# Kernel tuning notes

Measured on AMD Instinct MI355X. Metric: run time of the kernel, lower is better.

## Reference

```python
import jax, jax.numpy as jnp
import numpy as np

N = 50000      # nodes
E = 800000     # edges (before self loops)
IN = 256       # in_dim
HID = 32       # hidden_dim per head
H = 8          # heads layer 1
OUT = 64       # out_dim (classes)
NEG_SLOPE = 0.2  # PyG GATConv default


def gat_conv(x, ei, W, a_src, a_dst, b, heads, ch, concat):
    """PyG GATConv (eval mode, self-loops already in ei).
    x: [n, f_in], ei: [2, e] (row0=src j, row1=dst i), W: [f_in, heads*ch],
    a_src/a_dst: [heads, ch], b: [heads*ch] or [ch]."""
    n = x.shape[0]
    h = (x @ W).reshape(n, heads, ch)                      # [n, H, C]
    src, dst = ei[0], ei[1]
    alpha_src = (h * a_src).sum(-1)                        # [n, H]
    alpha_dst = (h * a_dst).sum(-1)                        # [n, H]
    e = jax.nn.leaky_relu(alpha_src[src] + alpha_dst[dst], NEG_SLOPE)  # [e, H]
    # segment softmax over incoming edges of each dst node
    emax = jax.lax.stop_gradient(jax.ops.segment_max(e, dst, num_segments=n))
    p = jnp.exp(e - emax[dst])
    denom = jax.ops.segment_sum(p, dst, num_segments=n)    # [n, H] (>0: self loops)
    alpha = p / denom[dst]                                 # [e, H]
    out = jax.ops.segment_sum(h[src] * alpha[:, :, None], dst, num_segments=n)  # [n, H, C]
    out = out.reshape(n, heads * ch) if concat else out.mean(axis=1)
    return out + b


def setup_inputs() -> dict:
    key = jax.random.key(0)
    ks = jax.random.split(key, 9)
    x = jax.random.normal(ks[0], (N, IN), jnp.float32)
    edge_index = jax.random.randint(ks[1], (2, E), 0, N, jnp.int32)
    W1 = jax.random.normal(ks[2], (IN, H * HID), jnp.float32) * 0.05
    a_src1 = jax.random.normal(ks[3], (H, HID), jnp.float32) * 0.1
    a_dst1 = jax.random.normal(ks[4], (H, HID), jnp.float32) * 0.1
    b1 = jnp.zeros((H * HID,), jnp.float32)
    W2 = jax.random.normal(ks[5], (H * HID, OUT), jnp.float32) * 0.05
    a_src2 = jax.random.normal(ks[6], (1, OUT), jnp.float32) * 0.1
    a_dst2 = jax.random.normal(ks[7], (1, OUT), jnp.float32) * 0.1
    b2 = jnp.zeros((OUT,), jnp.float32)
    return {"x": x, "edge_index": edge_index, "W1": W1, "a_src1": a_src1,
            "a_dst1": a_dst1, "b1": b1, "W2": W2, "a_src2": a_src2,
            "a_dst2": a_dst2, "b2": b2}


def reference(x, edge_index, W1, a_src1, a_dst1, b1, W2, a_src2, a_dst2, b2):
    n = x.shape[0]
    loops = jnp.arange(n, dtype=edge_index.dtype)
    ei = jnp.concatenate([edge_index, jnp.stack([loops, loops])], axis=1)  # add self loops
    h = gat_conv(x, ei, W1, a_src1, a_dst1, b1, H, HID, concat=True)
    h = jax.nn.relu(h)
    h = gat_conv(h, ei, W2, a_src2, a_dst2, b2, 1, OUT, concat=False)
    return jax.nn.log_softmax(h, axis=1)
```

## Files before the change

### kernel.cpp

```cpp
#include <hip/hip_runtime.h>
#include <math.h>

#define NNODES 50000
#define EORIG  800000
#define ETOT   850000
#define NBUCK  196
#define BSTRIDE 5120
#define P2CHUNK 4096
#define NBLK2  ((ETOT + P2CHUNK - 1)/P2CHUNK)

typedef __attribute__((ext_vector_type(8))) short bf8_t;
typedef __attribute__((ext_vector_type(4))) float f4_t;
typedef __attribute__((ext_vector_type(2))) float f2_t;

constexpr float LOG2E = 1.44269504f;

constexpr size_t align256(size_t x){ return (x + 255) & ~size_t(255); }
constexpr size_t OFF_OFFSETS = 0;
constexpr size_t OFF_DEG     = OFF_OFFSETS + align256((size_t)NNODES*4);
constexpr size_t OFF_GCUR    = OFF_DEG     + align256((size_t)NNODES*4);
constexpr size_t OFF_EPACK   = OFF_GCUR    + align256(NBUCK*4);
constexpr size_t OFF_SRC     = OFF_EPACK   + align256((size_t)NBUCK*BSTRIDE*4);
constexpr size_t OFF_AS1     = OFF_SRC     + align256((size_t)NBUCK*BSTRIDE*4);
constexpr size_t OFF_AD1     = OFF_AS1     + align256((size_t)NNODES*8*4);
constexpr size_t OFF_W1T     = OFF_AD1     + align256((size_t)NNODES*8*4);
constexpr size_t OFF_W2T     = OFF_W1T     + align256(256*256*2);
constexpr size_t OFF_H1F8    = OFF_W2T     + align256(64*256*2);
constexpr size_t OFF_OUT1B   = OFF_H1F8    + align256((size_t)NNODES*256);
constexpr size_t OFF_H2B     = OFF_H1F8;
constexpr size_t OFF_AS2     = OFF_OUT1B   + align256((size_t)NNODES*256*2);
constexpr size_t OFF_AD2     = OFF_AS2     + align256((size_t)NNODES*4);

__device__ __forceinline__ unsigned short f2bf(float f){
    union { float f; unsigned u; } v; v.f = f;
    unsigned r = v.u + 0x7FFF + ((v.u >> 16) & 1);
    return (unsigned short)(r >> 16);
}
__device__ __forceinline__ float bf2f(unsigned short s){
    union { unsigned u; float f; } v; v.u = ((unsigned)s) << 16;
    return v.f;
}


__global__ __launch_bounds__(256) void p3_part(const int* __restrict__ ei, int* __restrict__ gcur,
                                               int* __restrict__ epack){
    __shared__ int h[NBUCK];
    __shared__ int r[NBUCK];
    const int t = threadIdx.x;
    for (int i = t; i < NBUCK; i += 256){ h[i] = 0; r[i] = 0; }
    __syncthreads();
    const int base = blockIdx.x * P2CHUNK;
    int srcs[P2CHUNK/256], dsts[P2CHUNK/256];
#pragma unroll
    for (int j = 0; j < P2CHUNK/256; j++){
        int e = base + j*256 + t;
        if (e < ETOT){
            if (e < EORIG){ srcs[j] = ei[e]; dsts[j] = ei[EORIG + e]; }
            else          { srcs[j] = dsts[j] = e - EORIG; }
            atomicAdd(&h[dsts[j] >> 8], 1);
        } else dsts[j] = -1;
    }
    __syncthreads();
    for (int i = t; i < NBUCK; i += 256){
        int c = h[i];
        h[i] = c ? atomicAdd(&gcur[i], c) : 0;
    }
    __syncthreads();
#pragma unroll
    for (int j = 0; j < P2CHUNK/256; j++){
        if (dsts[j] >= 0){
            int b = dsts[j] >> 8;
            int rk = atomicAdd(&r[b], 1);
            epack[h[b] + rk] = (srcs[j] << 8) | (dsts[j] & 255);
        }
    }
}

__global__ __launch_bounds__(256) void p4_csr(const int* __restrict__ gcur, const int* __restrict__ epack,
                                              int* __restrict__ offsets, int* __restrict__ deg_g,
                                              int* __restrict__ srclist){
    __shared__ int deg[256];
    __shared__ int sm[256];
    __shared__ int cur[256];
    const int b = blockIdx.x, t = threadIdx.x;
    const int s0 = b * BSTRIDE, s1 = gcur[b];
    deg[t] = 0; __syncthreads();
    for (int i = s0 + t; i < s1; i += 256) atomicAdd(&deg[epack[i] & 255], 1);
    __syncthreads();
    int v = deg[t];
    sm[t] = v; __syncthreads();
    for (int off = 1; off < 256; off <<= 1){
        int add = (t >= off) ? sm[t-off] : 0;
        __syncthreads();
        sm[t] += add;
        __syncthreads();
    }
    int excl = sm[t] - v;
    int node = (b << 8) + t;
    if (node < NNODES){ offsets[node] = s0 + excl; deg_g[node] = v; }
    cur[t] = s0 + excl;
    __syncthreads();
    for (int i = s0 + t; i < s1; i += 256){
        int p = epack[i];
        int pos = atomicAdd(&cur[p & 255], 1);
        srclist[pos] = p >> 8;
    }
}


__global__ __launch_bounds__(256) void conv_w_k(const float* __restrict__ W1, const float* __restrict__ W2,
                                                short* __restrict__ w1t, short* __restrict__ w2t,
                                                int* __restrict__ gcur){
    int o = blockIdx.x*256 + threadIdx.x;
    if (o < NBUCK) gcur[o] = o * BSTRIDE;
    if (o < 256*256){
        int n = o >> 8, k = o & 255;
        w1t[o] = (short)f2bf(W1[k*256 + n]);
    } else {
        int o2 = o - 256*256;
        if (o2 < 64*256){
            int n = o2 >> 8, k = o2 & 255;
            w2t[o2] = (short)f2bf(W2[k*64 + n]);
        }
    }
}


__global__ __launch_bounds__(512) void gemm1_mfma(const float* __restrict__ x, const short* __restrict__ w1t,
        const float* __restrict__ a1s, const float* __restrict__ a1d,
        unsigned char* __restrict__ h1f8, float* __restrict__ as1, float* __restrict__ ad1){
    __shared__ short As[128][40];
    __shared__ short Bs[256][40];
    const int t = threadIdx.x;
    const int lane = t & 63, wave = t >> 6;
    const int wy = wave >> 2, wx = wave & 3;
    const int quad = lane >> 4, l15 = lane & 15;
    const int r0 = blockIdx.x * 128;
    const int srow = t >> 2, skoff = (t & 3) * 8;
    f4_t zero4 = {0.f,0.f,0.f,0.f};
    f4_t acc[4][4];
#pragma unroll
    for (int i=0;i<4;i++)
#pragma unroll
      for (int j=0;j<4;j++) acc[i][j] = zero4;

    for (int kk = 0; kk < 256; kk += 32){
        float4 xa0 = {0,0,0,0}, xa1 = {0,0,0,0};
        if (r0 + srow < NNODES){
            xa0 = *(const float4*)(x + (size_t)(r0+srow)*256 + kk + skoff);
            xa1 = *(const float4*)(x + (size_t)(r0+srow)*256 + kk + skoff + 4);
        }
        bf8_t b0  = *(const bf8_t*)(w1t + (size_t)(srow      )*256 + kk + skoff);
        bf8_t b1v = *(const bf8_t*)(w1t + (size_t)(srow + 128)*256 + kk + skoff);
        bf8_t a0;
        a0[0]=f2bf(xa0.x); a0[1]=f2bf(xa0.y); a0[2]=f2bf(xa0.z); a0[3]=f2bf(xa0.w);
        a0[4]=f2bf(xa1.x); a0[5]=f2bf(xa1.y); a0[6]=f2bf(xa1.z); a0[7]=f2bf(xa1.w);
        __syncthreads();
        *(bf8_t*)&As[srow     ][skoff] = a0;
        *(bf8_t*)&Bs[srow     ][skoff] = b0;
        *(bf8_t*)&Bs[srow+128][skoff] = b1v;
        __syncthreads();
        bf8_t af[4], bfr[4];
#pragma unroll
        for (int i=0;i<4;i++) af[i]  = *(const bf8_t*)&As[wy*64 + i*16 + l15][quad*8];
#pragma unroll
        for (int j=0;j<4;j++) bfr[j] = *(const bf8_t*)&Bs[wx*64 + j*16 + l15][quad*8];
#pragma unroll
        for (int i=0;i<4;i++)
#pragma unroll
          for (int j=0;j<4;j++)
            acc[i][j] = __builtin_amdgcn_mfma_f32_16x16x32_bf16(af[i], bfr[j], acc[i][j], 0,0,0);
    }
    const int colbase = wx*64;
    const int head0 = colbase >> 5;
    float cs[4], cd[4];
#pragma unroll
    for (int j=0;j<4;j++){
        cs[j] = a1s[colbase + j*16 + l15] * LOG2E;
        cd[j] = a1d[colbase + j*16 + l15] * LOG2E;
    }
#pragma unroll
    for (int i=0;i<4;i++){
        int rowb = r0 + wy*64 + i*16 + quad*4;
#pragma unroll
        for (int reg=0; reg<4; reg++){
            int row = rowb + reg;
            bool valid = row < NNODES;
            float sp0=0.f, dp0=0.f, sp1=0.f, dp1=0.f;
#pragma unroll
            for (int j=0;j<4;j++){
                float v = acc[i][j][reg];
                if (j < 2){ sp0 += v*cs[j]; dp0 += v*cd[j]; }
                else      { sp1 += v*cs[j]; dp1 += v*cd[j]; }
                if (valid){
                    unsigned enc = (unsigned)__builtin_amdgcn_cvt_pk_fp8_f32(v, v, 0, false);
                    h1f8[(size_t)row*256 + colbase + j*16 + l15] = (unsigned char)(enc & 0xffu);
                }
            }
            sp0 += __shfl_xor(sp0,1); sp0 += __shfl_xor(sp0,2); sp0 += __shfl_xor(sp0,4); sp0 += __shfl_xor(sp0,8);
            dp0 += __shfl_xor(dp0,1); dp0 += __shfl_xor(dp0,2); dp0 += __shfl_xor(dp0,4); dp0 += __shfl_xor(dp0,8);
            sp1 += __shfl_xor(sp1,1); sp1 += __shfl_xor(sp1,2); sp1 += __shfl_xor(sp1,4); sp1 += __shfl_xor(sp1,8);
            dp1 += __shfl_xor(dp1,1); dp1 += __shfl_xor(dp1,2); dp1 += __shfl_xor(dp1,4); dp1 += __shfl_xor(dp1,8);
            if (valid && l15 == 0){
                as1[row*8 + head0    ] = sp0;
                ad1[row*8 + head0    ] = dp0;
                as1[row*8 + head0 + 1] = sp1;
                ad1[row*8 + head0 + 1] = dp1;
            }
        }
    }
}


__global__ __launch_bounds__(256) void gemm2_mfma(const short* __restrict__ ab, const short* __restrict__ w2t,
        const float* __restrict__ a2s, const float* __restrict__ a2d,
        short* __restrict__ h2b, float* __restrict__ as2, float* __restrict__ ad2){
    __shared__ short As[128][40];
    __shared__ short Bs[64][40];
    const int t = threadIdx.x;
    const int lane = t & 63, wave = t >> 6;
    const int quad = lane >> 4, l15 = lane & 15;
    const int r0 = blockIdx.x * 128;
    const int srow = t >> 2, skoff = (t & 3) * 8;
    f4_t zero4 = {0.f,0.f,0.f,0.f};
    f4_t acc[2][4];
#pragma unroll
    for (int i=0;i<2;i++)
#pragma unroll
      for (int j=0;j<4;j++) acc[i][j] = zero4;

    for (int kk = 0; kk < 256; kk += 32){
        bf8_t a0 = {}, a1v = {};
        if (r0 + srow < NNODES)      a0  = *(const bf8_t*)(ab + (size_t)(r0+srow)*256 + kk + skoff);
        if (r0 + srow + 64 < NNODES) a1v = *(const bf8_t*)(ab + (size_t)(r0+srow+64)*256 + kk + skoff);
        bf8_t b0 = *(const bf8_t*)(w2t + (size_t)srow*256 + kk + skoff);
        __syncthreads();
        *(bf8_t*)&As[srow   ][skoff] = a0;
        *(bf8_t*)&As[srow+64][skoff] = a1v;
        *(bf8_t*)&Bs[srow   ][skoff] = b0;
        __syncthreads();
        bf8_t af[2], bfr[4];
#pragma unroll
        for (int i=0;i<2;i++) af[i]  = *(const bf8_t*)&As[wave*32 + i*16 + l15][quad*8];
#pragma unroll
        for (int j=0;j<4;j++) bfr[j] = *(const bf8_t*)&Bs[j*16 + l15][quad*8];
#pragma unroll
        for (int i=0;i<2;i++)
#pragma unroll
          for (int j=0;j<4;j++)
            acc[i][j] = __builtin_amdgcn_mfma_f32_16x16x32_bf16(af[i], bfr[j], acc[i][j], 0,0,0);
    }
    float cs[4], cd[4];
#pragma unroll
    for (int j=0;j<4;j++){
        cs[j] = a2s[j*16 + l15] * LOG2E;
        cd[j] = a2d[j*16 + l15] * LOG2E;
    }
#pragma unroll
    for (int i=0;i<2;i++){
        int rowb = r0 + wave*32 + i*16 + quad*4;
#pragma unroll
        for (int reg=0; reg<4; reg++){
            int row = rowb + reg;
            bool valid = row < NNODES;
            float sp=0.f, dp=0.f;
#pragma unroll
            for (int j=0;j<4;j++){
                float v = acc[i][j][reg];
                sp += v*cs[j]; dp += v*cd[j];
                if (valid) h2b[(size_t)row*64 + j*16 + l15] = (short)f2bf(v);
            }
            sp += __shfl_xor(sp,1); sp += __shfl_xor(sp,2); sp += __shfl_xor(sp,4); sp += __shfl_xor(sp,8);
            dp += __shfl_xor(dp,1); dp += __shfl_xor(dp,2); dp += __shfl_xor(dp,4); dp += __shfl_xor(dp,8);
            if (valid && l15 == 0){ as2[row] = sp; ad2[row] = dp; }
        }
    }
}


__global__ __launch_bounds__(256) void aggregate1_k(const unsigned char* __restrict__ h1f8,
        const float* __restrict__ as1, const float* __restrict__ ad1,
        const int* __restrict__ offsets, const int* __restrict__ deg_g,
        const int* __restrict__ srclist,
        const float* __restrict__ b1, short* __restrict__ out1b){
    int d = blockIdx.x*4 + (threadIdx.x >> 6);
    int lane = threadIdx.x & 63;
    if (d >= NNODES) return;
    const int sub    = lane >> 4;
    const int c16    = lane & 15;
    const int head_g = c16 >> 1;
    const int head_p = lane & 7;
    const int ep     = lane >> 3;
    int start = offsets[d];
    int deg = deg_g[d];
    float ad_p = ad1[d*8 + head_p];
    float denom = 0.f;
    f2_t acc[8];
#pragma unroll
    for (int i=0;i<8;i++) acc[i] = (f2_t){0.f,0.f};
    for (int w = 0; w < deg; w += 64){
        int deg_w = min(64, deg - w);
        int s_reg = srclist[start + w + min(lane, deg_w-1)];
        int ngr = (deg_w + 7) >> 3;
        auto comp_p = [&](int g)->float{
            int ei = g*8 + ep;
            int s  = __shfl(s_reg, min(ei, deg_w-1));
            float e = as1[s*8 + head_p] + ad_p;
            e = fmaxf(0.2f*e, e);
            float p = exp2f(e);
            return (ei < deg_w) ? p : 0.f;
        };
        float p_reg = comp_p(0);
        for (int g = 0; g < ngr; g++){
            float p_cur = p_reg;
            if (g + 1 < ngr) p_reg = comp_p(g+1);
#pragma unroll
            for (int q = 0; q < 2; q++){
                int eq = q*4 + sub;
                float pe = __shfl(p_cur, eq*8 + head_g);
                int   se = __shfl(s_reg, g*8 + eq);
                uint4 wv = *(const uint4*)(h1f8 + (size_t)se*256 + c16*16);
                f2_t v;
                v = __builtin_amdgcn_cvt_pk_f32_fp8(wv.x, false); acc[0] += pe*v;
                v = __builtin_amdgcn_cvt_pk_f32_fp8(wv.x, true);  acc[1] += pe*v;
                v = __builtin_amdgcn_cvt_pk_f32_fp8(wv.y, false); acc[2] += pe*v;
                v = __builtin_amdgcn_cvt_pk_f32_fp8(wv.y, true);  acc[3] += pe*v;
                v = __builtin_amdgcn_cvt_pk_f32_fp8(wv.z, false); acc[4] += pe*v;
                v = __builtin_amdgcn_cvt_pk_f32_fp8(wv.z, true);  acc[5] += pe*v;
                v = __builtin_amdgcn_cvt_pk_f32_fp8(wv.w, false); acc[6] += pe*v;
                v = __builtin_amdgcn_cvt_pk_f32_fp8(wv.w, true);  acc[7] += pe*v;
                denom += pe;
            }
        }
    }
#pragma unroll
    for (int i=0;i<8;i++){
        acc[i][0] += __shfl_xor(acc[i][0], 16);
        acc[i][1] += __shfl_xor(acc[i][1], 16);
        acc[i][0] += __shfl_xor(acc[i][0], 32);
        acc[i][1] += __shfl_xor(acc[i][1], 32);
    }
    denom += __shfl_xor(denom, 16);
    denom += __shfl_xor(denom, 32);
    if (sub == 0){
        float inv = 1.f / denom;
        const float4 bv0 = *(const float4*)(b1 + c16*16);
        const float4 bv1 = *(const float4*)(b1 + c16*16 + 4);
        const float4 bv2 = *(const float4*)(b1 + c16*16 + 8);
        const float4 bv3 = *(const float4*)(b1 + c16*16 + 12);
        bf8_t r0, r1;
        r0[0] = (short)f2bf(fmaxf(acc[0][0]*inv + bv0.x, 0.f));
        r0[1] = (short)f2bf(fmaxf(acc[0][1]*inv + bv0.y, 0.f));
        r0[2] = (short)f2bf(fmaxf(acc[1][0]*inv + bv0.z, 0.f));
        r0[3] = (short)f2bf(fmaxf(acc[1][1]*inv + bv0.w, 0.f));
        r0[4] = (short)f2bf(fmaxf(acc[2][0]*inv + bv1.x, 0.f));
        r0[5] = (short)f2bf(fmaxf(acc[2][1]*inv + bv1.y, 0.f));
        r0[6] = (short)f2bf(fmaxf(acc[3][0]*inv + bv1.z, 0.f));
        r0[7] = (short)f2bf(fmaxf(acc[3][1]*inv + bv1.w, 0.f));
        r1[0] = (short)f2bf(fmaxf(acc[4][0]*inv + bv2.x, 0.f));
        r1[1] = (short)f2bf(fmaxf(acc[4][1]*inv + bv2.y, 0.f));
        r1[2] = (short)f2bf(fmaxf(acc[5][0]*inv + bv2.z, 0.f));
        r1[3] = (short)f2bf(fmaxf(acc[5][1]*inv + bv2.w, 0.f));
        r1[4] = (short)f2bf(fmaxf(acc[6][0]*inv + bv3.x, 0.f));
        r1[5] = (short)f2bf(fmaxf(acc[6][1]*inv + bv3.y, 0.f));
        r1[6] = (short)f2bf(fmaxf(acc[7][0]*inv + bv3.z, 0.f));
        r1[7] = (short)f2bf(fmaxf(acc[7][1]*inv + bv3.w, 0.f));
        *(bf8_t*)(out1b + (size_t)d*256 + c16*16)     = r0;
        *(bf8_t*)(out1b + (size_t)d*256 + c16*16 + 8) = r1;
    }
}

__global__ __launch_bounds__(256) void aggregate2_k(const unsigned short* __restrict__ h2b,
        const float* __restrict__ as2, const float* __restrict__ ad2,
        const int* __restrict__ offsets, const int* __restrict__ deg_g,
        const int* __restrict__ srclist,
        const float* __restrict__ b2, float* __restrict__ out){
    int d = blockIdx.x*4 + (threadIdx.x >> 6);
    int lane = threadIdx.x & 63;
    if (d >= NNODES) return;
    const int sub = lane >> 3;
    const int c8  = lane & 7;
    int start = offsets[d];
    int deg = deg_g[d];
    float ad_v = ad2[d];
    float denom = 0.f;
    float accv[8] = {0.f,0.f,0.f,0.f,0.f,0.f,0.f,0.f};
    for (int w = 0; w < deg; w += 64){
        int deg_w = min(64, deg - w);
        int s_reg = srclist[start + w + min(lane, deg_w-1)];
        float ev = as2[s_reg] + ad_v;
        ev = fmaxf(0.2f*ev, ev);
        float p_lane = (lane < deg_w) ? exp2f(ev) : 0.f;
        int ngr = (deg_w + 7) >> 3;
        for (int g = 0; g < ngr; g++){
            int eq = g*8 + sub;
            float pe = __shfl(p_lane, eq);
            int   se = __shfl(s_reg, eq);
            bf8_t hv = *(const bf8_t*)(h2b + (size_t)se*64 + c8*8);
#pragma unroll
            for (int k=0;k<8;k++) accv[k] += pe * bf2f((unsigned short)hv[k]);
            denom += pe;
        }
    }
#pragma unroll
    for (int k=0;k<8;k++){
        accv[k] += __shfl_xor(accv[k], 8);
        accv[k] += __shfl_xor(accv[k], 16);
        accv[k] += __shfl_xor(accv[k], 32);
    }
    denom += __shfl_xor(denom, 8);
    denom += __shfl_xor(denom, 16);
    denom += __shfl_xor(denom, 32);
    float inv = 1.f / denom;
    float v[8];
    float mx = -1e30f;
#pragma unroll
    for (int k=0;k<8;k++){
        v[k] = accv[k]*inv + b2[c8*8 + k];
        mx = fmaxf(mx, v[k]);
    }
    mx = fmaxf(mx, __shfl_xor(mx, 1));
    mx = fmaxf(mx, __shfl_xor(mx, 2));
    mx = fmaxf(mx, __shfl_xor(mx, 4));
    float ss = 0.f;
#pragma unroll
    for (int k=0;k<8;k++) ss += __expf(v[k] - mx);
    ss += __shfl_xor(ss, 1);
    ss += __shfl_xor(ss, 2);
    ss += __shfl_xor(ss, 4);
    if (sub == 0){
        float lg = mx + __logf(ss);
        float4 o0 = {v[0]-lg, v[1]-lg, v[2]-lg, v[3]-lg};
        float4 o1 = {v[4]-lg, v[5]-lg, v[6]-lg, v[7]-lg};
        *(float4*)(out + (size_t)d*64 + c8*8)     = o0;
        *(float4*)(out + (size_t)d*64 + c8*8 + 4) = o1;
    }
}


extern "C" void kernel_launch(void* const* d_in, const int* in_sizes, int n_in,
                              void* d_out, int out_size, void* d_ws, size_t ws_size,
                              hipStream_t stream){
    const float* x      = (const float*)d_in[0];
    const int*   ei     = (const int*)  d_in[1];
    const float* W1     = (const float*)d_in[2];
    const float* a_src1 = (const float*)d_in[3];
    const float* a_dst1 = (const float*)d_in[4];
    const float* b1     = (const float*)d_in[5];
    const float* W2     = (const float*)d_in[6];
    const float* a_src2 = (const float*)d_in[7];
    const float* a_dst2 = (const float*)d_in[8];
    const float* b2     = (const float*)d_in[9];

    char* ws = (char*)d_ws;
    int*   offsets = (int*)  (ws + OFF_OFFSETS);
    int*   deg_g   = (int*)  (ws + OFF_DEG);
    int*   gcur    = (int*)  (ws + OFF_GCUR);
    int*   epack   = (int*)  (ws + OFF_EPACK);
    int*   srclist = (int*)  (ws + OFF_SRC);
    float* as1     = (float*)(ws + OFF_AS1);
    float* ad1     = (float*)(ws + OFF_AD1);
    short* w1t     = (short*)(ws + OFF_W1T);
    short* w2t     = (short*)(ws + OFF_W2T);
    unsigned char* h1f8 = (unsigned char*)(ws + OFF_H1F8);
    short* out1b   = (short*)(ws + OFF_OUT1B);
    short* h2b     = (short*)(ws + OFF_H2B);
    float* as2     = (float*)(ws + OFF_AS2);
    float* ad2     = (float*)(ws + OFF_AD2);

    conv_w_k<<<(256*256 + 64*256 + 255)/256, 256, 0, stream>>>(W1, W2, w1t, w2t, gcur);

    p3_part<<<NBLK2, 256, 0, stream>>>(ei, gcur, epack);
    p4_csr <<<NBUCK, 256, 0, stream>>>(gcur, epack, offsets, deg_g, srclist);

    gemm1_mfma<<<(NNODES+127)/128, 512, 0, stream>>>(x, w1t, a_src1, a_dst1, h1f8, as1, ad1);
    aggregate1_k<<<(NNODES+3)/4, 256, 0, stream>>>(h1f8, as1, ad1, offsets, deg_g, srclist, b1, out1b);

    gemm2_mfma<<<(NNODES+127)/128, 256, 0, stream>>>(out1b, w2t, a_src2, a_dst2, h2b, as2, ad2);
    aggregate2_k<<<(NNODES+3)/4, 256, 0, stream>>>((const unsigned short*)h2b, as2, ad2, offsets, deg_g, srclist, b2, (float*)d_out);
}
```

Measured before the change: 249.1 us.

## Double-buffer GEMM A tiles in LDS and load weight fragments directly from global

Both dense GEMMs now use 64-row tiles, with the A tile double-buffered in shared memory so the next K slice is fetched while MFMAs run on the current one. Weight fragments skip LDS and are loaded straight from global (L2-resident) into registers, also prefetched one step ahead. This leaves one barrier per K step instead of two and makes the grid larger for better occupancy and load balance. In exchange, every wave reads its weights from global memory, which raises L2 traffic, and more register pressure comes from the prefetch buffers.

```diff
diff --git a/kernel.cpp b/kernel.cpp
--- a/kernel.cpp
+++ b/kernel.cpp
@@ -126,17 +126,18 @@
 }
 
 
-__global__ __launch_bounds__(512) void gemm1_mfma(const float* __restrict__ x, const short* __restrict__ w1t,
+__global__ __launch_bounds__(256) void gemm1_mfma(const float* __restrict__ x, const short* __restrict__ w1t,
         const float* __restrict__ a1s, const float* __restrict__ a1d,
         unsigned char* __restrict__ h1f8, float* __restrict__ as1, float* __restrict__ ad1){
-    __shared__ short As[128][40];
-    __shared__ short Bs[256][40];
+    __shared__ short As[2][64][40];
     const int t = threadIdx.x;
     const int lane = t & 63, wave = t >> 6;
-    const int wy = wave >> 2, wx = wave & 3;
     const int quad = lane >> 4, l15 = lane & 15;
-    const int r0 = blockIdx.x * 128;
+    const int r0 = blockIdx.x * 64;
     const int srow = t >> 2, skoff = (t & 3) * 8;
+    const bool arow_ok = (r0 + srow) < NNODES;
+    const float* xrow = x + (size_t)(r0 + srow)*256 + skoff;
+    const short* wbase = w1t + (size_t)(wave*64 + l15)*256 + quad*8;
     f4_t zero4 = {0.f,0.f,0.f,0.f};
     f4_t acc[4][4];
 #pragma unroll
@@ -144,34 +145,47 @@
 #pragma unroll
       for (int j=0;j<4;j++) acc[i][j] = zero4;
 
-    for (int kk = 0; kk < 256; kk += 32){
-        float4 xa0 = {0,0,0,0}, xa1 = {0,0,0,0};
-        if (r0 + srow < NNODES){
-            xa0 = *(const float4*)(x + (size_t)(r0+srow)*256 + kk + skoff);
-            xa1 = *(const float4*)(x + (size_t)(r0+srow)*256 + kk + skoff + 4);
-        }
-        bf8_t b0  = *(const bf8_t*)(w1t + (size_t)(srow      )*256 + kk + skoff);
-        bf8_t b1v = *(const bf8_t*)(w1t + (size_t)(srow + 128)*256 + kk + skoff);
+    float4 xa0 = {0,0,0,0}, xa1 = {0,0,0,0};
+    if (arow_ok){ xa0 = *(const float4*)(xrow); xa1 = *(const float4*)(xrow + 4); }
+    bf8_t bcur[4], bnxt[4];
+#pragma unroll
+    for (int j=0;j<4;j++) bcur[j] = *(const bf8_t*)(wbase + j*16*256);
+    {
         bf8_t a0;
         a0[0]=f2bf(xa0.x); a0[1]=f2bf(xa0.y); a0[2]=f2bf(xa0.z); a0[3]=f2bf(xa0.w);
         a0[4]=f2bf(xa1.x); a0[5]=f2bf(xa1.y); a0[6]=f2bf(xa1.z); a0[7]=f2bf(xa1.w);
-        __syncthreads();
-        *(bf8_t*)&As[srow     ][skoff] = a0;
-        *(bf8_t*)&Bs[srow     ][skoff] = b0;
-        *(bf8_t*)&Bs[srow+128][skoff] = b1v;
-        __syncthreads();
-        bf8_t af[4], bfr[4];
-#pragma unroll
-        for (int i=0;i<4;i++) af[i]  = *(const bf8_t*)&As[wy*64 + i*16 + l15][quad*8];
-#pragma unroll
-        for (int j=0;j<4;j++) bfr[j] = *(const bf8_t*)&Bs[wx*64 + j*16 + l15][quad*8];
+        *(bf8_t*)&As[0][srow][skoff] = a0;
+    }
+    __syncthreads();
+    int cur = 0;
+#pragma unroll
+    for (int s = 0; s < 8; s++){
+        if (s < 7){
+            const int kn = s*32 + 32;
+            if (arow_ok){ xa0 = *(const float4*)(xrow + kn); xa1 = *(const float4*)(xrow + kn + 4); }
+#pragma unroll
+            for (int j=0;j<4;j++) bnxt[j] = *(const bf8_t*)(wbase + j*16*256 + kn);
+        }
+        bf8_t af[4];
+#pragma unroll
+        for (int i=0;i<4;i++) af[i] = *(const bf8_t*)&As[cur][i*16 + l15][quad*8];
 #pragma unroll
         for (int i=0;i<4;i++)
 #pragma unroll
           for (int j=0;j<4;j++)
-            acc[i][j] = __builtin_amdgcn_mfma_f32_16x16x32_bf16(af[i], bfr[j], acc[i][j], 0,0,0);
-    }
-    const int colbase = wx*64;
+            acc[i][j] = __builtin_amdgcn_mfma_f32_16x16x32_bf16(af[i], bcur[j], acc[i][j], 0,0,0);
+        if (s < 7){
+            bf8_t a0;
+            a0[0]=f2bf(xa0.x); a0[1]=f2bf(xa0.y); a0[2]=f2bf(xa0.z); a0[3]=f2bf(xa0.w);
+            a0[4]=f2bf(xa1.x); a0[5]=f2bf(xa1.y); a0[6]=f2bf(xa1.z); a0[7]=f2bf(xa1.w);
+            *(bf8_t*)&As[cur^1][srow][skoff] = a0;
+            __syncthreads();
+            cur ^= 1;
+#pragma unroll
+            for (int j=0;j<4;j++) bcur[j] = bnxt[j];
+        }
+    }
+    const int colbase = wave*64;
     const int head0 = colbase >> 5;
     float cs[4], cd[4];
 #pragma unroll
@@ -181,7 +195,7 @@
     }
 #pragma unroll
     for (int i=0;i<4;i++){
-        int rowb = r0 + wy*64 + i*16 + quad*4;
+        int rowb = r0 + i*16 + quad*4;
 #pragma unroll
         for (int reg=0; reg<4; reg++){
             int row = rowb + reg;
@@ -215,40 +229,48 @@
 __global__ __launch_bounds__(256) void gemm2_mfma(const short* __restrict__ ab, const short* __restrict__ w2t,
         const float* __restrict__ a2s, const float* __restrict__ a2d,
         short* __restrict__ h2b, float* __restrict__ as2, float* __restrict__ ad2){
-    __shared__ short As[128][40];
-    __shared__ short Bs[64][40];
+    __shared__ short As[2][64][40];
     const int t = threadIdx.x;
     const int lane = t & 63, wave = t >> 6;
     const int quad = lane >> 4, l15 = lane & 15;
-    const int r0 = blockIdx.x * 128;
+    const int r0 = blockIdx.x * 64;
     const int srow = t >> 2, skoff = (t & 3) * 8;
+    const bool arow_ok = (r0 + srow) < NNODES;
+    const short* arow = ab + (size_t)(r0 + srow)*256 + skoff;
+    const short* wbase = w2t + (size_t)l15*256 + quad*8;
     f4_t zero4 = {0.f,0.f,0.f,0.f};
-    f4_t acc[2][4];
-#pragma unroll
-    for (int i=0;i<2;i++)
-#pragma unroll
-      for (int j=0;j<4;j++) acc[i][j] = zero4;
-
-    for (int kk = 0; kk < 256; kk += 32){
-        bf8_t a0 = {}, a1v = {};
-        if (r0 + srow < NNODES)      a0  = *(const bf8_t*)(ab + (size_t)(r0+srow)*256 + kk + skoff);
-        if (r0 + srow + 64 < NNODES) a1v = *(const bf8_t*)(ab + (size_t)(r0+srow+64)*256 + kk + skoff);
-        bf8_t b0 = *(const bf8_t*)(w2t + (size_t)srow*256 + kk + skoff);
-        __syncthreads();
-        *(bf8_t*)&As[srow   ][skoff] = a0;
-        *(bf8_t*)&As[srow+64][skoff] = a1v;
-        *(bf8_t*)&Bs[srow   ][skoff] = b0;
-        __syncthreads();
-        bf8_t af[2], bfr[4];
-#pragma unroll
-        for (int i=0;i<2;i++) af[i]  = *(const bf8_t*)&As[wave*32 + i*16 + l15][quad*8];
-#pragma unroll
-        for (int j=0;j<4;j++) bfr[j] = *(const bf8_t*)&Bs[j*16 + l15][quad*8];
-#pragma unroll
-        for (int i=0;i<2;i++)
-#pragma unroll
-          for (int j=0;j<4;j++)
-            acc[i][j] = __builtin_amdgcn_mfma_f32_16x16x32_bf16(af[i], bfr[j], acc[i][j], 0,0,0);
+    f4_t acc[4];
+#pragma unroll
+    for (int j=0;j<4;j++) acc[j] = zero4;
+
+    bf8_t a0 = {};
+    if (arow_ok) a0 = *(const bf8_t*)(arow);
+    bf8_t bcur[4], bnxt[4];
+#pragma unroll
+    for (int j=0;j<4;j++) bcur[j] = *(const bf8_t*)(wbase + j*16*256);
+    *(bf8_t*)&As[0][srow][skoff] = a0;
+    __syncthreads();
+    int cur = 0;
+#pragma unroll
+    for (int s = 0; s < 8; s++){
+        bf8_t anx = {};
+        if (s < 7){
+            const int kn = s*32 + 32;
+            if (arow_ok) anx = *(const bf8_t*)(arow + kn);
+#pragma unroll
+            for (int j=0;j<4;j++) bnxt[j] = *(const bf8_t*)(wbase + j*16*256 + kn);
+        }
+        bf8_t af = *(const bf8_t*)&As[cur][wave*16 + l15][quad*8];
+#pragma unroll
+        for (int j=0;j<4;j++)
+            acc[j] = __builtin_amdgcn_mfma_f32_16x16x32_bf16(af, bcur[j], acc[j], 0,0,0);
+        if (s < 7){
+            *(bf8_t*)&As[cur^1][srow][skoff] = anx;
+            __syncthreads();
+            cur ^= 1;
+#pragma unroll
+            for (int j=0;j<4;j++) bcur[j] = bnxt[j];
+        }
     }
     float cs[4], cd[4];
 #pragma unroll
@@ -256,24 +278,21 @@
         cs[j] = a2s[j*16 + l15] * LOG2E;
         cd[j] = a2d[j*16 + l15] * LOG2E;
     }
-#pragma unroll
-    for (int i=0;i<2;i++){
-        int rowb = r0 + wave*32 + i*16 + quad*4;
-#pragma unroll
-        for (int reg=0; reg<4; reg++){
-            int row = rowb + reg;
-            bool valid = row < NNODES;
-            float sp=0.f, dp=0.f;
-#pragma unroll
-            for (int j=0;j<4;j++){
-                float v = acc[i][j][reg];
-                sp += v*cs[j]; dp += v*cd[j];
-                if (valid) h2b[(size_t)row*64 + j*16 + l15] = (short)f2bf(v);
-            }
-            sp += __shfl_xor(sp,1); sp += __shfl_xor(sp,2); sp += __shfl_xor(sp,4); sp += __shfl_xor(sp,8);
-            dp += __shfl_xor(dp,1); dp += __shfl_xor(dp,2); dp += __shfl_xor(dp,4); dp += __shfl_xor(dp,8);
-            if (valid && l15 == 0){ as2[row] = sp; ad2[row] = dp; }
-        }
+    int rowb = r0 + wave*16 + quad*4;
+#pragma unroll
+    for (int reg=0; reg<4; reg++){
+        int row = rowb + reg;
+        bool valid = row < NNODES;
+        float sp=0.f, dp=0.f;
+#pragma unroll
+        for (int j=0;j<4;j++){
+            float v = acc[j][reg];
+            sp += v*cs[j]; dp += v*cd[j];
+            if (valid) h2b[(size_t)row*64 + j*16 + l15] = (short)f2bf(v);
+        }
+        sp += __shfl_xor(sp,1); sp += __shfl_xor(sp,2); sp += __shfl_xor(sp,4); sp += __shfl_xor(sp,8);
+        dp += __shfl_xor(dp,1); dp += __shfl_xor(dp,2); dp += __shfl_xor(dp,4); dp += __shfl_xor(dp,8);
+        if (valid && l15 == 0){ as2[row] = sp; ad2[row] = dp; }
     }
 }
 
@@ -473,9 +492,9 @@
     p3_part<<<NBLK2, 256, 0, stream>>>(ei, gcur, epack);
     p4_csr <<<NBUCK, 256, 0, stream>>>(gcur, epack, offsets, deg_g, srclist);
 
-    gemm1_mfma<<<(NNODES+127)/128, 512, 0, stream>>>(x, w1t, a_src1, a_dst1, h1f8, as1, ad1);
+    gemm1_mfma<<<(NNODES+63)/64, 256, 0, stream>>>(x, w1t, a_src1, a_dst1, h1f8, as1, ad1);
     aggregate1_k<<<(NNODES+3)/4, 256, 0, stream>>>(h1f8, as1, ad1, offsets, deg_g, srclist, b1, out1b);
 
-    gemm2_mfma<<<(NNODES+127)/128, 256, 0, stream>>>(out1b, w2t, a_src2, a_dst2, h2b, as2, ad2);
+    gemm2_mfma<<<(NNODES+63)/64, 256, 0, stream>>>(out1b, w2t, a_src2, a_dst2, h2b, as2, ad2);
     aggregate2_k<<<(NNODES+3)/4, 256, 0, stream>>>((const unsigned short*)h2b, as2, ad2, offsets, deg_g, srclist, b2, (float*)d_out);
 }
```

Measured after the change: 257.6 us. 3.4% more time.
